# Kernel tuning notes

Hardware: AMD Instinct MI355X
Metric: run time of the kernel (lower is better)

Reference implementation:

```python
import jax, jax.numpy as jnp
import numpy as np

B, S, D = 2, 2048, 2048
H, KVH, HD = 16, 4, 128
THETA = 10000.0
NEG = -1e9


def _rope_tables(seq_len, head_dim, theta, batch):
    inv_freq = 1.0 / (theta ** (np.arange(0, head_dim, 2, dtype=np.float32) / head_dim))
    t = np.arange(seq_len, dtype=np.float32)
    freqs = np.outer(t, inv_freq)                      # (S, HD/2)
    emb = np.concatenate([freqs, freqs], axis=-1)      # (S, HD)
    cos = np.broadcast_to(np.cos(emb), (batch, seq_len, head_dim))
    sin = np.broadcast_to(np.sin(emb), (batch, seq_len, head_dim))
    return jnp.asarray(cos), jnp.asarray(sin)


def setup_inputs() -> dict:
    key = jax.random.key(0)
    ks = jax.random.split(key, 5)
    hidden_states = jax.random.normal(ks[0], (B, S, D), dtype=jnp.float32)
    cos, sin = _rope_tables(S, HD, THETA, B)
    # additive causal mask (B, 1, S, S)
    causal = jnp.where(jnp.tril(jnp.ones((S, S), dtype=bool)), 0.0, NEG).astype(jnp.float32)
    attention_mask = jnp.broadcast_to(causal[None, None], (B, 1, S, S))
    sc = 0.02
    Wq = jax.random.normal(ks[1], (H * HD, D), dtype=jnp.float32) * sc
    Wk = jax.random.normal(ks[2], (KVH * HD, D), dtype=jnp.float32) * sc
    Wv = jax.random.normal(ks[3], (KVH * HD, D), dtype=jnp.float32) * sc
    Wo = jax.random.normal(ks[4], (D, H * HD), dtype=jnp.float32) * sc
    return {"hidden_states": hidden_states, "cos": cos, "sin": sin,
            "attention_mask": attention_mask, "Wq": Wq, "Wk": Wk, "Wv": Wv, "Wo": Wo}


def _rotate_half(x):
    h = x.shape[-1] // 2
    return jnp.concatenate([-x[..., h:], x[..., :h]], axis=-1)


def _apply_rope(x, cos, sin):
    # x: (B, nH, S, HD); cos/sin: (B, S, HD) -> broadcast over heads
    c = cos[:, None, :, :]
    s = sin[:, None, :, :]
    return x * c + _rotate_half(x) * s


def reference(hidden_states, cos, sin, attention_mask, Wq, Wk, Wv, Wo):
    b, s, _ = hidden_states.shape
    q = (hidden_states @ Wq.T).reshape(b, s, H, HD).transpose(0, 2, 1, 3)    # (B,H,S,HD)
    k = (hidden_states @ Wk.T).reshape(b, s, KVH, HD).transpose(0, 2, 1, 3)  # (B,KVH,S,HD)
    v = (hidden_states @ Wv.T).reshape(b, s, KVH, HD).transpose(0, 2, 1, 3)
    q = _apply_rope(q, cos, sin)
    k = _apply_rope(k, cos, sin)
    groups = H // KVH
    k = jnp.repeat(k, groups, axis=1)  # (B,H,S,HD)
    v = jnp.repeat(v, groups, axis=1)
    scaling = HD ** -0.5
    scores = jnp.einsum('bhqd,bhkd->bhqk', q, k) * scaling
    scores = scores + attention_mask[:, :, :, :s]
    attn_weights = jax.nn.softmax(scores.astype(jnp.float32), axis=-1).astype(q.dtype)
    attn_out = jnp.einsum('bhqk,bhkd->bhqd', attn_weights, v)
    attn_out = attn_out.transpose(0, 2, 1, 3).reshape(b, s, H * HD)
    attn_out = attn_out @ Wo.T
    return attn_out, attn_weights
```

## Files before the change

kernel.cpp:

```cpp
#include <hip/hip_runtime.h>
#include <hip/hip_bf16.h>
#include <stdint.h>

#define B_ 2
#define S_ 2048
#define D_ 2048
#define H_ 16
#define KVH_ 4
#define HD_ 128
#define SCALE_ 0.08838834764831845f

typedef _Float16 f16;
typedef __attribute__((ext_vector_type(8))) _Float16 f16x8;
typedef __attribute__((ext_vector_type(4))) _Float16 f16x4;
typedef __attribute__((ext_vector_type(4))) float   f32x4;

#define MFMA16(a, b, c) __builtin_amdgcn_mfma_f32_16x16x32_f16((a), (b), (c), 0, 0, 0)

__device__ __forceinline__ void gload16(const void* g, void* l) {
  __builtin_amdgcn_global_load_lds(
      (const __attribute__((address_space(1))) void*)g,
      (__attribute__((address_space(3))) void*)l, 16, 0, 0);
}

__global__ void cvt_kernel(const float* __restrict__ src, f16* __restrict__ dst, int n4) {
  int i = blockIdx.x * 256 + threadIdx.x;
  int stride = gridDim.x * 256;
  for (; i < n4; i += stride) {
    float4 v = ((const float4*)src)[i];
    f16x4 h = { (f16)v.x, (f16)v.y, (f16)v.z, (f16)v.w };
    ((f16x4*)dst)[i] = h;
  }
}

template <int OUTF16>
__global__ __launch_bounds__(256, 2) void gemm_nt(const f16* __restrict__ A,
                                                  const f16* __restrict__ Bm,
                                                  void* __restrict__ Cout,
                                                  int M, int N, int K) {
  __shared__ f16 Alds[128 * 32];
  __shared__ f16 Blds[128 * 32];
  const int t = threadIdx.x, w = t >> 6, l = t & 63;
  const int g = l >> 4, lo = l & 15;
  const int tm = blockIdx.x * 128, tn = blockIdx.y * 128;
  const int wr = w >> 1, wc = w & 1;

  f32x4 acc[4][4];
#pragma unroll
  for (int mi = 0; mi < 4; mi++)
#pragma unroll
    for (int ni = 0; ni < 4; ni++) acc[mi][ni] = (f32x4){0.f, 0.f, 0.f, 0.f};

  const int NT = K >> 5;
  auto stage = [&](int kt) {
    const int kb = kt * 32;
#pragma unroll
    for (int i = 0; i < 2; i++) {
      int chunk = w * 2 + i;
      int row = chunk * 16 + (l >> 2);
      int kh = (l & 3) * 8;
      gload16(A + (size_t)(tm + row) * K + kb + kh, Alds + chunk * 512);
      gload16(Bm + (size_t)(tn + row) * K + kb + kh, Blds + chunk * 512);
    }
  };

  stage(0);
  for (int kt = 0; kt < NT; ++kt) {
    __syncthreads();
    f16x8 af[4], bf[4];
#pragma unroll
    for (int mi = 0; mi < 4; mi++)
      af[mi] = *(const f16x8*)(Alds + (wr * 64 + mi * 16 + lo) * 32 + g * 8);
#pragma unroll
    for (int ni = 0; ni < 4; ni++)
      bf[ni] = *(const f16x8*)(Blds + (wc * 64 + ni * 16 + lo) * 32 + g * 8);
#pragma unroll
    for (int mi = 0; mi < 4; mi++)
#pragma unroll
      for (int ni = 0; ni < 4; ni++)
        acc[mi][ni] = MFMA16(af[mi], bf[ni], acc[mi][ni]);
    __syncthreads();
    if (kt + 1 < NT) stage(kt + 1);
  }

#pragma unroll
  for (int mi = 0; mi < 4; mi++)
#pragma unroll
    for (int ni = 0; ni < 4; ni++)
#pragma unroll
      for (int r = 0; r < 4; r++) {
        int row = tm + wr * 64 + mi * 16 + g * 4 + r;
        int col = tn + wc * 64 + ni * 16 + lo;
        if (OUTF16)
          ((f16*)Cout)[(size_t)row * N + col] = (f16)acc[mi][ni][r];
        else
          ((float*)Cout)[(size_t)row * N + col] = acc[mi][ni][r];
      }
}

__global__ void rope_kernel(const f16* __restrict__ qkv, const float* __restrict__ cosb,
                            const float* __restrict__ sinb, f16* __restrict__ Qro,
                            f16* __restrict__ Kro, f16* __restrict__ Vtr) {
  const int row = blockIdx.x;
  const int b = row >> 11, s = row & 2047;
  const float* cp = cosb + ((size_t)b * S_ + s) * HD_;
  const float* sp = sinb + ((size_t)b * S_ + s) * HD_;
  const f16* src = qkv + (size_t)row * 3072;
  for (int i = threadIdx.x; i < 1280; i += 256) {
    int hh = i >> 6, d = i & 63;
    float c = cp[d], sn = sp[d];
    float x0 = (float)src[hh * 128 + d];
    float x1 = (float)src[hh * 128 + d + 64];
    float o0 = x0 * c - x1 * sn;
    float o1 = x1 * c + x0 * sn;
    f16* dst;
    if (hh < 16)
      dst = Qro + (((size_t)b * H_ + hh) * S_ + s) * HD_;
    else
      dst = Kro + (((size_t)b * KVH_ + (hh - 16)) * S_ + s) * HD_;
    dst[d] = (f16)o0;
    dst[d + 64] = (f16)o1;
  }
  for (int i = threadIdx.x; i < 512; i += 256) {
    int hh = i >> 7, d = i & 127;
    Vtr[(((size_t)b * KVH_ + hh) * HD_ + d) * S_ + s] = src[2560 + hh * 128 + d];
  }
}

__global__ __launch_bounds__(256, 2) void attn_pass1(const f16* __restrict__ Qro,
                                                     const f16* __restrict__ Kro,
                                                     const f16* __restrict__ Vtr,
                                                     f16* __restrict__ attn16,
                                                     float* __restrict__ rowsum) {
  const int qi = blockIdx.x, h = blockIdx.y, b = blockIdx.z;
  const int kvh = h >> 2;
  const int t = threadIdx.x, w = t >> 6, l = t & 63, g = l >> 4, lo = l & 15;
  __shared__ f16 Klds[64 * 128];
  __shared__ f16 Vlds[128 * 64];
  __shared__ f16 Wlds[128 * 72];
  const f16* Qb = Qro + (((size_t)b * H_ + h) * S_ + qi * 128) * HD_;
  const f16* Kb = Kro + ((size_t)b * KVH_ + kvh) * S_ * HD_;
  const f16* Vb = Vtr + ((size_t)b * KVH_ + kvh) * HD_ * S_;

  f16x8 qf[2][4];
#pragma unroll
  for (int mi = 0; mi < 2; mi++)
#pragma unroll
    for (int kk = 0; kk < 4; kk++)
      qf[mi][kk] = *(const f16x8*)(Qb + (size_t)(w * 32 + mi * 16 + lo) * HD_ + kk * 32 + g * 8);

  f32x4 o[2][8];
#pragma unroll
  for (int mi = 0; mi < 2; mi++)
#pragma unroll
    for (int no = 0; no < 8; no++) o[mi][no] = (f32x4){0.f, 0.f, 0.f, 0.f};
  float rs[2][4] = {{0.f, 0.f, 0.f, 0.f}, {0.f, 0.f, 0.f, 0.f}};

  const int jmax = 2 * qi + 1;
  for (int j = 0; j <= jmax; ++j) {
    __syncthreads();
#pragma unroll
    for (int i = 0; i < 4; i++) {
      int chunk = w * 4 + i;
      {
        int row = chunk * 4 + (l >> 4);
        int cb = ((l & 15) * 16) ^ ((row & 7) << 4);
        gload16(Kb + (size_t)(j * 64 + row) * HD_ + (cb >> 1), Klds + chunk * 512);
      }
      {
        int row = chunk * 8 + (l >> 3);
        int cb = ((l & 7) * 16) ^ ((row & 7) << 4);
        gload16(Vb + (size_t)row * S_ + j * 64 + (cb >> 1), Vlds + chunk * 512);
      }
    }
    __syncthreads();

    f32x4 sa[2][4];
#pragma unroll
    for (int mi = 0; mi < 2; mi++)
#pragma unroll
      for (int ni = 0; ni < 4; ni++) sa[mi][ni] = (f32x4){0.f, 0.f, 0.f, 0.f};
#pragma unroll
    for (int kk = 0; kk < 4; kk++) {
      f16x8 kf[4];
#pragma unroll
      for (int ni = 0; ni < 4; ni++) {
        int row = ni * 16 + lo;
        int kb2 = (kk * 64 + g * 16) ^ ((row & 7) << 4);
        kf[ni] = *(const f16x8*)(Klds + row * 128 + (kb2 >> 1));
      }
#pragma unroll
      for (int mi = 0; mi < 2; mi++)
#pragma unroll
        for (int ni = 0; ni < 4; ni++)
          sa[mi][ni] = MFMA16(qf[mi][kk], kf[ni], sa[mi][ni]);
    }

    const bool partial = (j >= 2 * qi);
#pragma unroll
    for (int mi = 0; mi < 2; mi++) {
      float part[4] = {0.f, 0.f, 0.f, 0.f};
#pragma unroll
      for (int ni = 0; ni < 4; ni++)
#pragma unroll
        for (int r = 0; r < 4; r++) {
          int qrow = qi * 128 + w * 32 + mi * 16 + g * 4 + r;
          int kcol = j * 64 + ni * 16 + lo;
          float e = __expf(sa[mi][ni][r] * SCALE_);
          if (partial && kcol > qrow) e = 0.f;
          part[r] += e;
          Wlds[(w * 32 + mi * 16 + g * 4 + r) * 72 + ni * 16 + lo] = (f16)e;
        }
#pragma unroll
      for (int r = 0; r < 4; r++) {
        float v = part[r];
        v += __shfl_xor(v, 1);
        v += __shfl_xor(v, 2);
        v += __shfl_xor(v, 4);
        v += __shfl_xor(v, 8);
        rs[mi][r] += v;
      }
    }

#pragma unroll
    for (int kk2 = 0; kk2 < 2; kk2++) {
      f16x8 wa[2], vb[8];
#pragma unroll
      for (int mi = 0; mi < 2; mi++)
        wa[mi] = *(const f16x8*)(Wlds + (w * 32 + mi * 16 + lo) * 72 + kk2 * 32 + g * 8);
#pragma unroll
      for (int no = 0; no < 8; no++) {
        int row = no * 16 + lo;
        int kb2 = (kk2 * 64 + g * 16) ^ ((row & 7) << 4);
        vb[no] = *(const f16x8*)(Vlds + row * 64 + (kb2 >> 1));
      }
#pragma unroll
      for (int mi = 0; mi < 2; mi++)
#pragma unroll
        for (int no = 0; no < 8; no++)
          o[mi][no] = MFMA16(wa[mi], vb[no], o[mi][no]);
    }
  }

#pragma unroll
  for (int mi = 0; mi < 2; mi++) {
    float inv[4];
#pragma unroll
    for (int r = 0; r < 4; r++) inv[r] = 1.f / rs[mi][r];
#pragma unroll
    for (int no = 0; no < 8; no++)
#pragma unroll
      for (int r = 0; r < 4; r++) {
        int srow = qi * 128 + w * 32 + mi * 16 + g * 4 + r;
        attn16[((size_t)b * S_ + srow) * (H_ * HD_) + h * HD_ + no * 16 + lo] =
            (f16)(o[mi][no][r] * inv[r]);
      }
  }
  if (lo == 0) {
#pragma unroll
    for (int mi = 0; mi < 2; mi++)
#pragma unroll
      for (int r = 0; r < 4; r++)
        rowsum[((size_t)b * H_ + h) * S_ + qi * 128 + w * 32 + mi * 16 + g * 4 + r] =
            rs[mi][r];
  }
}

__global__ __launch_bounds__(256, 2) void attn_pass2(const f16* __restrict__ Qro,
                                                     const f16* __restrict__ Kro,
                                                     const float* __restrict__ rowsum,
                                                     float* __restrict__ wout) {
  const int qi = blockIdx.x, h = blockIdx.y, b = blockIdx.z;
  const int kvh = h >> 2;
  const int t = threadIdx.x, w = t >> 6, l = t & 63, g = l >> 4, lo = l & 15;
  __shared__ f16 Klds[64 * 128];
  const f16* Qb = Qro + (((size_t)b * H_ + h) * S_ + qi * 128) * HD_;
  const f16* Kb = Kro + ((size_t)b * KVH_ + kvh) * S_ * HD_;

  f16x8 qf[2][4];
#pragma unroll
  for (int mi = 0; mi < 2; mi++)
#pragma unroll
    for (int kk = 0; kk < 4; kk++)
      qf[mi][kk] = *(const f16x8*)(Qb + (size_t)(w * 32 + mi * 16 + lo) * HD_ + kk * 32 + g * 8);

  float inv[2][4];
#pragma unroll
  for (int mi = 0; mi < 2; mi++)
#pragma unroll
    for (int r = 0; r < 4; r++)
      inv[mi][r] = 1.f / rowsum[((size_t)b * H_ + h) * S_ + qi * 128 + w * 32 + mi * 16 + g * 4 + r];

  float* wb = wout + (((size_t)b * H_ + h) * S_ + qi * 128) * S_;
  const int jmax = 2 * qi + 1;
  for (int j = 0; j < S_ / 64; ++j) {
    if (j <= jmax) {
      __syncthreads();
#pragma unroll
      for (int i = 0; i < 4; i++) {
        int chunk = w * 4 + i;
        int row = chunk * 4 + (l >> 4);
        int cb = ((l & 15) * 16) ^ ((row & 7) << 4);
        gload16(Kb + (size_t)(j * 64 + row) * HD_ + (cb >> 1), Klds + chunk * 512);
      }
      __syncthreads();
      f32x4 sa[2][4];
#pragma unroll
      for (int mi = 0; mi < 2; mi++)
#pragma unroll
        for (int ni = 0; ni < 4; ni++) sa[mi][ni] = (f32x4){0.f, 0.f, 0.f, 0.f};
#pragma unroll
      for (int kk = 0; kk < 4; kk++) {
        f16x8 kf[4];
#pragma unroll
        for (int ni = 0; ni < 4; ni++) {
          int row = ni * 16 + lo;
          int kb2 = (kk * 64 + g * 16) ^ ((row & 7) << 4);
          kf[ni] = *(const f16x8*)(Klds + row * 128 + (kb2 >> 1));
        }
#pragma unroll
        for (int mi = 0; mi < 2; mi++)
#pragma unroll
          for (int ni = 0; ni < 4; ni++)
            sa[mi][ni] = MFMA16(qf[mi][kk], kf[ni], sa[mi][ni]);
      }
      const bool partial = (j >= 2 * qi);
#pragma unroll
      for (int mi = 0; mi < 2; mi++)
#pragma unroll
        for (int ni = 0; ni < 4; ni++)
#pragma unroll
          for (int r = 0; r < 4; r++) {
            int qrl = w * 32 + mi * 16 + g * 4 + r;
            int kcol = j * 64 + ni * 16 + lo;
            float e = __expf(sa[mi][ni][r] * SCALE_) * inv[mi][r];
            if (partial && kcol > qi * 128 + qrl) e = 0.f;
            wb[(size_t)qrl * S_ + kcol] = e;
          }
    } else {
      for (int i = t; i < 2048; i += 256) {
        int row = i >> 4, c = i & 15;
        *(float4*)(wb + (size_t)row * S_ + j * 64 + c * 4) = make_float4(0.f, 0.f, 0.f, 0.f);
      }
    }
  }
}

extern "C" void kernel_launch(void* const* d_in, const int* in_sizes, int n_in,
                              void* d_out, int out_size, void* d_ws, size_t ws_size,
                              hipStream_t stream) {
  (void)in_sizes; (void)n_in; (void)out_size; (void)ws_size;
  const float* hidden = (const float*)d_in[0];
  const float* cosb   = (const float*)d_in[1];
  const float* sinb   = (const float*)d_in[2];
  const float* Wq = (const float*)d_in[4];
  const float* Wk = (const float*)d_in[5];
  const float* Wv = (const float*)d_in[6];
  const float* Wo = (const float*)d_in[7];

  char* ws = (char*)d_ws;
  f16* hidden16 = (f16*)ws; ws += (size_t)4096 * 2048 * 2;
  f16* W16      = (f16*)ws; ws += (size_t)3072 * 2048 * 2;
  f16* Wo16     = (f16*)ws; ws += (size_t)2048 * 2048 * 2;
  f16* qkv16    = (f16*)ws; ws += (size_t)4096 * 3072 * 2;
  f16* Qro      = (f16*)ws; ws += (size_t)B_ * H_ * S_ * HD_ * 2;
  f16* Kro      = (f16*)ws; ws += (size_t)B_ * KVH_ * S_ * HD_ * 2;
  f16* Vtr      = (f16*)ws; ws += (size_t)B_ * KVH_ * S_ * HD_ * 2;
  f16* attn16   = (f16*)ws; ws += (size_t)4096 * 2048 * 2;
  float* rowsum = (float*)ws; ws += (size_t)B_ * H_ * S_ * 4;

  float* out_attn = (float*)d_out;
  float* out_w    = (float*)d_out + (size_t)B_ * S_ * D_;

  cvt_kernel<<<2048, 256, 0, stream>>>(hidden, hidden16, 4096 * 2048 / 4);
  cvt_kernel<<<1024, 256, 0, stream>>>(Wq, W16, 2048 * 2048 / 4);
  cvt_kernel<<<256, 256, 0, stream>>>(Wk, W16 + (size_t)2048 * 2048, 512 * 2048 / 4);
  cvt_kernel<<<256, 256, 0, stream>>>(Wv, W16 + (size_t)2560 * 2048, 512 * 2048 / 4);
  cvt_kernel<<<1024, 256, 0, stream>>>(Wo, Wo16, 2048 * 2048 / 4);

  gemm_nt<1><<<dim3(32, 24), 256, 0, stream>>>(hidden16, W16, qkv16, 4096, 3072, 2048);
  rope_kernel<<<4096, 256, 0, stream>>>(qkv16, cosb, sinb, Qro, Kro, Vtr);
  attn_pass1<<<dim3(16, 16, 2), 256, 0, stream>>>(Qro, Kro, Vtr, attn16, rowsum);
  gemm_nt<0><<<dim3(32, 16), 256, 0, stream>>>(attn16, Wo16, out_attn, 4096, 2048, 2048);
  attn_pass2<<<dim3(16, 16, 2), 256, 0, stream>>>(Qro, Kro, rowsum, out_w);
}
```

Baseline: 924.7 us.

## Use 256x256 double-buffered swizzled GEMM, merge conversions, balance causal attention blocks

Replaces the 128x128 single-buffered GEMM with a 512-thread 256x256 tile GEMM. It double-buffers K-slices in LDS with XOR swizzling, waits on explicit vmcnt counts and raises MFMA priority, all to increase data reuse and overlap loads with compute. The five conversion launches are merged into one kernel, and attention blocks for batch 1 are ordered in reverse so causal work is spread more evenly. The risks are lower occupancy from 128 KB of LDS and fewer blocks (192 and 128 tiles) on a 256-CU part.

```diff
diff --git a/kernel.cpp b/kernel.cpp
--- a/kernel.cpp
+++ b/kernel.cpp
@@ -1,6 +1,7 @@
 #include <hip/hip_runtime.h>
 #include <hip/hip_bf16.h>
 #include <stdint.h>
+
 
 #define B_ 2
 #define S_ 2048
@@ -16,6 +17,9 @@
 typedef __attribute__((ext_vector_type(4))) float   f32x4;
 
 #define MFMA16(a, b, c) __builtin_amdgcn_mfma_f32_16x16x32_f16((a), (b), (c), 0, 0, 0)
+#define WAITVM4 asm volatile("s_waitcnt vmcnt(4)" ::: "memory")
+#define WAITVM0 asm volatile("s_waitcnt vmcnt(0)" ::: "memory")
+#define BAR     asm volatile("s_barrier" ::: "memory")
 
 __device__ __forceinline__ void gload16(const void* g, void* l) {
   __builtin_amdgcn_global_load_lds(
@@ -23,73 +27,138 @@
       (__attribute__((address_space(3))) void*)l, 16, 0, 0);
 }
 
-__global__ void cvt_kernel(const float* __restrict__ src, f16* __restrict__ dst, int n4) {
+__global__ void cvt_all(const float* __restrict__ h, const float* __restrict__ wq,
+                        const float* __restrict__ wk, const float* __restrict__ wv,
+                        const float* __restrict__ wo, f16* __restrict__ h16,
+                        f16* __restrict__ w16, f16* __restrict__ wo16) {
+  const int n_h = 2097152, n_q = 1048576, n_k = 262144, n_v = 262144;
+  const int total = 4718592;
   int i = blockIdx.x * 256 + threadIdx.x;
-  int stride = gridDim.x * 256;
-  for (; i < n4; i += stride) {
-    float4 v = ((const float4*)src)[i];
-    f16x4 h = { (f16)v.x, (f16)v.y, (f16)v.z, (f16)v.w };
-    ((f16x4*)dst)[i] = h;
+  const int stride = gridDim.x * 256;
+  for (; i < total; i += stride) {
+    const float* s; f16* d; int j = i;
+    if (j < n_h) { s = h; d = h16; }
+    else {
+      j -= n_h;
+      if (j < n_q) { s = wq; d = w16; }
+      else {
+        j -= n_q;
+        if (j < n_k) { s = wk; d = w16 + 4194304; }
+        else {
+          j -= n_k;
+          if (j < n_v) { s = wv; d = w16 + 5242880; }
+          else { j -= n_v; s = wo; d = wo16; }
+        }
+      }
+    }
+    float4 v = ((const float4*)s)[j];
+    f16x4 o = {(f16)v.x, (f16)v.y, (f16)v.z, (f16)v.w};
+    ((f16x4*)d)[j] = o;
   }
 }
 
 template <int OUTF16>
-__global__ __launch_bounds__(256, 2) void gemm_nt(const f16* __restrict__ A,
+__global__ __launch_bounds__(512, 2) void gemm256(const f16* __restrict__ A,
                                                   const f16* __restrict__ Bm,
                                                   void* __restrict__ Cout,
                                                   int M, int N, int K) {
-  __shared__ f16 Alds[128 * 32];
-  __shared__ f16 Blds[128 * 32];
-  const int t = threadIdx.x, w = t >> 6, l = t & 63;
+  __shared__ f16 lds[65536];
+  const int t_ = threadIdx.x, w = t_ >> 6, l = t_ & 63;
   const int g = l >> 4, lo = l & 15;
-  const int tm = blockIdx.x * 128, tn = blockIdx.y * 128;
-  const int wr = w >> 1, wc = w & 1;
-
-  f32x4 acc[4][4];
-#pragma unroll
-  for (int mi = 0; mi < 4; mi++)
+  const int wr = w >> 2, wc = w & 3;
+  const int tm = blockIdx.x * 256, tn = blockIdx.y * 256;
+  const int NT = K >> 6;
+
+  const int srow = w * 32 + (l >> 2);
+  const int schunk = (l & 3) ^ ((srow >> 1) & 3);
+  const f16* aS0 = A + (size_t)(tm + srow) * K + schunk * 8;
+  const f16* aS1 = aS0 + (size_t)16 * K;
+  const f16* bS0 = Bm + (size_t)(tn + srow) * K + schunk * 8;
+  const f16* bS1 = bS0 + (size_t)16 * K;
+
+  int aoff[8], boff[4];
+#pragma unroll
+  for (int mi = 0; mi < 8; mi++) {
+    int r_ = wr * 128 + mi * 16 + lo;
+    aoff[mi] = r_ * 32 + ((g ^ ((r_ >> 1) & 3)) << 3);
+  }
+#pragma unroll
+  for (int ni = 0; ni < 4; ni++) {
+    int r_ = wc * 64 + ni * 16 + lo;
+    boff[ni] = r_ * 32 + ((g ^ ((r_ >> 1) & 3)) << 3);
+  }
+
+  f32x4 acc[8][4];
+#pragma unroll
+  for (int mi = 0; mi < 8; mi++)
 #pragma unroll
     for (int ni = 0; ni < 4; ni++) acc[mi][ni] = (f32x4){0.f, 0.f, 0.f, 0.f};
 
-  const int NT = K >> 5;
-  auto stage = [&](int kt) {
-    const int kb = kt * 32;
-#pragma unroll
-    for (int i = 0; i < 2; i++) {
-      int chunk = w * 2 + i;
-      int row = chunk * 16 + (l >> 2);
-      int kh = (l & 3) * 8;
-      gload16(A + (size_t)(tm + row) * K + kb + kh, Alds + chunk * 512);
-      gload16(Bm + (size_t)(tn + row) * K + kb + kh, Blds + chunk * 512);
-    }
+  auto stage_kh = [&](int nbuf, int kh, int t) {
+    f16* la = lds + ((nbuf * 2 + 0) * 2 + kh) * 8192 + w * 1024;
+    f16* lb = lds + ((nbuf * 2 + 1) * 2 + kh) * 8192 + w * 1024;
+    const int ko = t * 64 + kh * 32;
+    gload16(aS0 + ko, la);
+    gload16(aS1 + ko, la + 512);
+    gload16(bS0 + ko, lb);
+    gload16(bS1 + ko, lb + 512);
   };
 
-  stage(0);
-  for (int kt = 0; kt < NT; ++kt) {
-    __syncthreads();
-    f16x8 af[4], bf[4];
-#pragma unroll
-    for (int mi = 0; mi < 4; mi++)
-      af[mi] = *(const f16x8*)(Alds + (wr * 64 + mi * 16 + lo) * 32 + g * 8);
+  stage_kh(0, 0, 0);
+  stage_kh(0, 1, 0);
+
+  int cb = 0;
+  for (int t = 0; t < NT; ++t, cb ^= 1) {
+    const bool stg = (t + 1 < NT);
+    WAITVM4;
+    BAR;
+    {
+      const f16* Ab = lds + ((cb * 2 + 0) * 2 + 0) * 8192;
+      const f16* Bb = lds + ((cb * 2 + 1) * 2 + 0) * 8192;
+      f16x8 a8[8], b8[4];
+#pragma unroll
+      for (int mi = 0; mi < 8; mi++) a8[mi] = *(const f16x8*)(Ab + aoff[mi]);
+#pragma unroll
+      for (int ni = 0; ni < 4; ni++) b8[ni] = *(const f16x8*)(Bb + boff[ni]);
+      if (stg) stage_kh(cb ^ 1, 0, t + 1);
+      BAR;
+      __builtin_amdgcn_s_setprio(1);
+#pragma unroll
+      for (int mi = 0; mi < 8; mi++)
+#pragma unroll
+        for (int ni = 0; ni < 4; ni++)
+          acc[mi][ni] = MFMA16(a8[mi], b8[ni], acc[mi][ni]);
+      __builtin_amdgcn_s_setprio(0);
+    }
+    if (t == NT - 1) { WAITVM0; } else { WAITVM4; }
+    BAR;
+    {
+      const f16* Ab = lds + ((cb * 2 + 0) * 2 + 1) * 8192;
+      const f16* Bb = lds + ((cb * 2 + 1) * 2 + 1) * 8192;
+      f16x8 a8[8], b8[4];
+#pragma unroll
+      for (int mi = 0; mi < 8; mi++) a8[mi] = *(const f16x8*)(Ab + aoff[mi]);
+#pragma unroll
+      for (int ni = 0; ni < 4; ni++) b8[ni] = *(const f16x8*)(Bb + boff[ni]);
+      if (stg) stage_kh(cb ^ 1, 1, t + 1);
+      BAR;
+      __builtin_amdgcn_s_setprio(1);
+#pragma unroll
+      for (int mi = 0; mi < 8; mi++)
+#pragma unroll
+        for (int ni = 0; ni < 4; ni++)
+          acc[mi][ni] = MFMA16(a8[mi], b8[ni], acc[mi][ni]);
+      __builtin_amdgcn_s_setprio(0);
+    }
+  }
+
+#pragma unroll
+  for (int mi = 0; mi < 8; mi++)
 #pragma unroll
     for (int ni = 0; ni < 4; ni++)
-      bf[ni] = *(const f16x8*)(Blds + (wc * 64 + ni * 16 + lo) * 32 + g * 8);
-#pragma unroll
-    for (int mi = 0; mi < 4; mi++)
-#pragma unroll
-      for (int ni = 0; ni < 4; ni++)
-        acc[mi][ni] = MFMA16(af[mi], bf[ni], acc[mi][ni]);
-    __syncthreads();
-    if (kt + 1 < NT) stage(kt + 1);
-  }
-
-#pragma unroll
-  for (int mi = 0; mi < 4; mi++)
-#pragma unroll
-    for (int ni = 0; ni < 4; ni++)
 #pragma unroll
       for (int r = 0; r < 4; r++) {
-        int row = tm + wr * 64 + mi * 16 + g * 4 + r;
+        int row = tm + wr * 128 + mi * 16 + g * 4 + r;
         int col = tn + wc * 64 + ni * 16 + lo;
         if (OUTF16)
           ((f16*)Cout)[(size_t)row * N + col] = (f16)acc[mi][ni][r];
@@ -132,7 +201,9 @@
                                                      const f16* __restrict__ Vtr,
                                                      f16* __restrict__ attn16,
                                                      float* __restrict__ rowsum) {
-  const int qi = blockIdx.x, h = blockIdx.y, b = blockIdx.z;
+  const int b = blockIdx.z;
+  const int qi = (b == 0) ? blockIdx.x : 15 - blockIdx.x;
+  const int h = blockIdx.y;
   const int kvh = h >> 2;
   const int t = threadIdx.x, w = t >> 6, l = t & 63, g = l >> 4, lo = l & 15;
   __shared__ f16 Klds[64 * 128];
@@ -270,7 +341,9 @@
                                                      const f16* __restrict__ Kro,
                                                      const float* __restrict__ rowsum,
                                                      float* __restrict__ wout) {
-  const int qi = blockIdx.x, h = blockIdx.y, b = blockIdx.z;
+  const int b = blockIdx.z;
+  const int qi = (b == 0) ? blockIdx.x : 15 - blockIdx.x;
+  const int h = blockIdx.y;
   const int kvh = h >> 2;
   const int t = threadIdx.x, w = t >> 6, l = t & 63, g = l >> 4, lo = l & 15;
   __shared__ f16 Klds[64 * 128];
@@ -372,15 +445,10 @@
   float* out_attn = (float*)d_out;
   float* out_w    = (float*)d_out + (size_t)B_ * S_ * D_;
 
-  cvt_kernel<<<2048, 256, 0, stream>>>(hidden, hidden16, 4096 * 2048 / 4);
-  cvt_kernel<<<1024, 256, 0, stream>>>(Wq, W16, 2048 * 2048 / 4);
-  cvt_kernel<<<256, 256, 0, stream>>>(Wk, W16 + (size_t)2048 * 2048, 512 * 2048 / 4);
-  cvt_kernel<<<256, 256, 0, stream>>>(Wv, W16 + (size_t)2560 * 2048, 512 * 2048 / 4);
-  cvt_kernel<<<1024, 256, 0, stream>>>(Wo, Wo16, 2048 * 2048 / 4);
-
-  gemm_nt<1><<<dim3(32, 24), 256, 0, stream>>>(hidden16, W16, qkv16, 4096, 3072, 2048);
+  cvt_all<<<2048, 256, 0, stream>>>(hidden, Wq, Wk, Wv, Wo, hidden16, W16, Wo16);
+  gemm256<1><<<dim3(16, 12), 512, 0, stream>>>(hidden16, W16, qkv16, 4096, 3072, 2048);
   rope_kernel<<<4096, 256, 0, stream>>>(qkv16, cosb, sinb, Qro, Kro, Vtr);
   attn_pass1<<<dim3(16, 16, 2), 256, 0, stream>>>(Qro, Kro, Vtr, attn16, rowsum);
-  gemm_nt<0><<<dim3(32, 16), 256, 0, stream>>>(attn16, Wo16, out_attn, 4096, 2048, 2048);
+  gemm256<0><<<dim3(16, 8), 512, 0, stream>>>(attn16, Wo16, out_attn, 4096, 2048, 2048);
   attn_pass2<<<dim3(16, 16, 2), 256, 0, stream>>>(Qro, Kro, rowsum, out_w);
 }
```

New measurement: 902.7 us. 1.02x faster.
